# Kernel optimization log

Hardware: AMD Instinct MI355X
Metric: run time of the kernel (lower is better)

The kernel has to match this reference:

```python
import jax, jax.numpy as jnp
import numpy as np

N = 100000
E = 3200000
IN_DIM = 128
HID = 64
BN_EPS = 1e-5


def _gcn_conv(x, W, b, src, dst, dinv):
    h = x @ W                                      # [N, out]
    coeff = (dinv[src] * dinv[dst])[:, None]       # [E, 1]
    msg = h[src] * coeff                           # gather over edges
    agg = jax.ops.segment_sum(msg, dst, num_segments=N)
    agg = agg + h * (dinv * dinv)[:, None]         # self-loop term
    return agg + b


def setup_inputs() -> dict:
    key = jax.random.key(0)
    ks = jax.random.split(key, 12)
    x = jax.random.normal(ks[0], (N, IN_DIM), dtype=jnp.float32)
    edge_index = jax.random.randint(ks[1], (2, E), 0, N, dtype=jnp.int64)
    s1 = 1.0 / np.sqrt(IN_DIM)
    s2 = 1.0 / np.sqrt(HID)
    W1 = jax.random.uniform(ks[2], (IN_DIM, HID), jnp.float32, -s1, s1)
    b1 = jnp.zeros((HID,), jnp.float32)
    W2 = jax.random.uniform(ks[3], (HID, HID), jnp.float32, -s2, s2)
    b2 = jnp.zeros((HID,), jnp.float32)
    W3 = jax.random.uniform(ks[4], (HID, 1), jnp.float32, -s2, s2)
    b3 = jnp.zeros((1,), jnp.float32)
    g1 = jnp.ones((HID,), jnp.float32)
    beta1 = jnp.zeros((HID,), jnp.float32)
    m1 = 0.1 * jax.random.normal(ks[5], (HID,), jnp.float32)
    v1 = jax.random.uniform(ks[6], (HID,), jnp.float32) + 0.5
    g2 = jnp.ones((HID,), jnp.float32)
    beta2 = jnp.zeros((HID,), jnp.float32)
    m2 = 0.1 * jax.random.normal(ks[7], (HID,), jnp.float32)
    v2 = jax.random.uniform(ks[8], (HID,), jnp.float32) + 0.5
    return {"x": x, "edge_index": edge_index,
            "W1": W1, "b1": b1, "W2": W2, "b2": b2, "W3": W3, "b3": b3,
            "g1": g1, "beta1": beta1, "m1": m1, "v1": v1,
            "g2": g2, "beta2": beta2, "m2": m2, "v2": v2}


def reference(x, edge_index, W1, b1, W2, b2, W3, b3,
              g1, beta1, m1, v1, g2, beta2, m2, v2):
    src, dst = edge_index[0], edge_index[1]
    # degree with self-loops (computed on destination index, PyG convention)
    deg = jax.ops.segment_sum(jnp.ones((E,), jnp.float32), dst, num_segments=N) + 1.0
    dinv = jax.lax.rsqrt(deg)

    def bn(h, g, beta, m, v):
        return (h - m) * jax.lax.rsqrt(v + BN_EPS) * g + beta

    h = _gcn_conv(x, W1, b1, src, dst, dinv)
    h = jax.nn.relu(bn(h, g1, beta1, m1, v1))  # dropout is a no-op in eval
    h = _gcn_conv(h, W2, b2, src, dst, dinv)
    h = jax.nn.relu(bn(h, g2, beta2, m2, v2))
    h = _gcn_conv(h, W3, b3, src, dst, dinv)
    return jax.nn.sigmoid(h)  # [N, 1]
```

## Files before the change

kernel.cpp:

```cpp
#include <hip/hip_runtime.h>
#include <math.h>

#define N_NODES 100000
#define E_EDGES 3200000
#define IN_DIM_ 128
#define HID_ 64
#define BN_EPS_ 1e-5f

#define PB 250
#define CHUNK 12800
#define NBUCK 391
#define BMAX 9600

typedef __attribute__((ext_vector_type(8))) short short8;
typedef __attribute__((ext_vector_type(4))) float f32x4;
typedef __attribute__((ext_vector_type(2))) float f32x2;

__device__ inline ushort f2bf(float f) {
    union { float f; unsigned u; } c; c.f = f;
    unsigned r = c.u + 0x7fff + ((c.u >> 16) & 1);
    return (ushort)(r >> 16);
}
__device__ inline f32x2 up2(unsigned u) {
    union { unsigned u; float f; } lo, hi;
    lo.u = u << 16; hi.u = u & 0xffff0000u;
    f32x2 r; r.x = lo.f; r.y = hi.f; return r;
}

__global__ __launch_bounds__(512) void passA1_hist(const int* __restrict__ ei,
                                                   int* __restrict__ histPB) {
    __shared__ int hist[NBUCK];
    int t = threadIdx.x, b = blockIdx.x;
    for (int k = t; k < NBUCK; k += 512) hist[k] = 0;
    __syncthreads();
    int e0 = b * CHUNK, e1 = e0 + CHUNK;
    for (int e = e0 + t; e < e1; e += 512) {
        int d = ei[E_EDGES + e];
        atomicAdd(&hist[d >> 8], 1);
    }
    __syncthreads();
    for (int k = t; k < NBUCK; k += 512) histPB[k * PB + b] = hist[k];
}

__global__ __launch_bounds__(256) void scan_rows(int* __restrict__ histPB,
                                                 int* __restrict__ bucket_tot) {
    __shared__ int wsum[4];
    int k = blockIdx.x, t = threadIdx.x, lane = t & 63, wv = t >> 6;
    int v = (t < PB) ? histPB[k * PB + t] : 0;
    int s = v;
#pragma unroll
    for (int off = 1; off < 64; off <<= 1) {
        int u = __shfl_up(s, off, 64);
        if (lane >= off) s += u;
    }
    if (lane == 63) wsum[wv] = s;
    __syncthreads();
    int wbase = 0;
    for (int w = 0; w < wv; w++) wbase += wsum[w];
    if (t < PB) histPB[k * PB + t] = wbase + s - v;
    if (t == 255) bucket_tot[k] = wbase + s;
}

__global__ __launch_bounds__(512) void scan_totals(const int* __restrict__ bucket_tot,
                                                   int* __restrict__ bucket_base,
                                                   int* __restrict__ row_ptr) {
    __shared__ int wsum[8];
    int t = threadIdx.x, lane = t & 63, wv = t >> 6;
    int v = (t < NBUCK) ? bucket_tot[t] : 0;
    int s = v;
#pragma unroll
    for (int off = 1; off < 64; off <<= 1) {
        int u = __shfl_up(s, off, 64);
        if (lane >= off) s += u;
    }
    if (lane == 63) wsum[wv] = s;
    __syncthreads();
    int wbase = 0;
    for (int w = 0; w < wv; w++) wbase += wsum[w];
    if (t < NBUCK) bucket_base[t] = wbase + s - v;
    if (t == 0) {
        bucket_base[NBUCK] = E_EDGES;
        row_ptr[N_NODES] = E_EDGES;
    }
}

__global__ __launch_bounds__(512) void passA2_sorted(const int* __restrict__ ei,
                                                     const int* __restrict__ histPB,
                                                     const int* __restrict__ bucket_base,
                                                     int* __restrict__ ebuf) {
    __shared__ int sorted[CHUNK];
    __shared__ ushort bid[CHUNK];
    __shared__ int cur[NBUCK];
    __shared__ int lbase[NBUCK];
    int t = threadIdx.x, b = blockIdx.x;
    for (int k = t; k < NBUCK; k += 512) cur[k] = 0;
    __syncthreads();
    int e0 = b * CHUNK;
    for (int e = e0 + t; e < e0 + CHUNK; e += 512)
        atomicAdd(&cur[ei[E_EDGES + e] >> 8], 1);
    __syncthreads();
    if (t < 64) {
        int run = 0;
        for (int c0 = 0; c0 < NBUCK; c0 += 64) {
            int idx = c0 + t;
            int v = (idx < NBUCK) ? cur[idx] : 0;
            int s = v;
#pragma unroll
            for (int off = 1; off < 64; off <<= 1) {
                int u = __shfl_up(s, off, 64);
                if (t >= off) s += u;
            }
            if (idx < NBUCK) lbase[idx] = run + s - v;
            run += __shfl(s, 63, 64);
        }
    }
    __syncthreads();
    for (int k = t; k < NBUCK; k += 512) cur[k] = lbase[k];
    __syncthreads();
    for (int e = e0 + t; e < e0 + CHUNK; e += 512) {
        int s = ei[e];
        int d = ei[E_EDGES + e];
        int k = d >> 8;
        int pos = atomicAdd(&cur[k], 1);
        sorted[pos] = s | ((d & 255) << 17);
        bid[pos] = (ushort)k;
    }
    __syncthreads();
    for (int j = t; j < CHUNK; j += 512) {
        int k = bid[j];
        int dest = bucket_base[k] + histPB[k * PB + b] + (j - lbase[k]);
        ebuf[dest] = sorted[j];
    }
}

__global__ __launch_bounds__(256) void passB_sorted(const int* __restrict__ ebuf,
                                                    const int* __restrict__ bucket_base,
                                                    int* __restrict__ row_ptr,
                                                    int* __restrict__ csr_src,
                                                    float* __restrict__ dinv) {
    __shared__ int sorted[BMAX];
    __shared__ int hist[256];
    __shared__ int wsum[4];
    int b = blockIdx.x, t = threadIdx.x, lane = t & 63, wv = t >> 6;
    int base = bucket_base[b], end = bucket_base[b + 1];
    hist[t] = 0;
    __syncthreads();
    for (int k = base + t; k < end; k += 256)
        atomicAdd(&hist[ebuf[k] >> 17], 1);
    __syncthreads();
    int v = hist[t];
    int s = v;
#pragma unroll
    for (int off = 1; off < 64; off <<= 1) {
        int u = __shfl_up(s, off, 64);
        if (lane >= off) s += u;
    }
    if (lane == 63) wsum[wv] = s;
    __syncthreads();
    int wbase = 0;
    for (int w = 0; w < wv; w++) wbase += wsum[w];
    int excl = wbase + s - v;
    int node = b * 256 + t;
    if (node < N_NODES) {
        row_ptr[node] = base + excl;
        dinv[node] = rsqrtf((float)v + 1.0f);
    }
    __syncthreads();
    hist[t] = excl;
    __syncthreads();
    for (int k = base + t; k < end; k += 256) {
        int pv = ebuf[k];
        int pos = atomicAdd(&hist[pv >> 17], 1);
        if (pos < BMAX) sorted[pos] = pv;
        else csr_src[base + pos] = pv & 0x1FFFF;
    }
    __syncthreads();
    int cnt = end - base;
    if (cnt > BMAX) cnt = BMAX;
    for (int j = t; j < cnt; j += 256)
        csr_src[base + j] = sorted[j] & 0x1FFFF;
}

__global__ __launch_bounds__(256) void sort_rows(const int* __restrict__ row_ptr,
                                                 int* __restrict__ csr_src) {
    int wv = (blockIdx.x * 256 + threadIdx.x) >> 6;
    int lane = threadIdx.x & 63;
    if (wv >= N_NODES) return;
    int beg = row_ptr[wv], end = row_ptr[wv + 1];
    int deg = end - beg;
    if (deg <= 1 || deg > 64) return;
    int val = (lane < deg) ? csr_src[beg + lane] : 0x7FFFFFFF;
#pragma unroll
    for (int k = 2; k <= 64; k <<= 1) {
#pragma unroll
        for (int j = 32; j > 0; j >>= 1) {
            if (j >= k) continue;
            int other = __shfl_xor(val, j, 64);
            bool lower = (lane & j) == 0;
            bool asc = (lane & k) == 0;
            int mn = min(val, other), mx = max(val, other);
            val = (lower == asc) ? mn : mx;
        }
    }
    if (lane < deg) csr_src[beg + lane] = val;
}

template<bool LAST>
__global__ __launch_bounds__(256) void gather_feat(const int* __restrict__ row_ptr,
                                                   const int* __restrict__ csr_src,
                                                   const ushort* __restrict__ hs,
                                                   const float* __restrict__ dinv,
                                                   const float* __restrict__ b,
                                                   const float* __restrict__ g,
                                                   const float* __restrict__ beta,
                                                   const float* __restrict__ m,
                                                   const float* __restrict__ v,
                                                   unsigned* __restrict__ y,
                                                   const float* __restrict__ W3,
                                                   float* __restrict__ hs3, int n) {
    int wave = (blockIdx.x * 256 + threadIdx.x) >> 6;
    if ((wave << 3) >= n) return;
    int l = threadIdx.x & 63;
    int es = l >> 3, fg = l & 7;
    int i = (wave << 3) + es;
    bool rowok = i < n;
    int ic = rowok ? i : (n - 1);

    const char* Hb = (const char*)hs;
    unsigned foff = (unsigned)fg << 4;
    unsigned zoff = ((unsigned)N_NODES << 7) + foff;

    f32x2 a01 = {0.f, 0.f}, a23 = {0.f, 0.f}, a45 = {0.f, 0.f}, a67 = {0.f, 0.f};

    {
        uint4 p = *(const uint4*)(Hb + (((unsigned)ic << 7) + foff));
        a01 += up2(p.x); a23 += up2(p.y); a45 += up2(p.z); a67 += up2(p.w);
    }

    int beg = row_ptr[ic], end = row_ptr[ic + 1];
    for (int k = beg; k < end; k += 8) {
        unsigned o[8];
#pragma unroll
        for (int j = 0; j < 8; j++) {
            int kj = k + j;
            int sj = csr_src[kj < end ? kj : k];
            o[j] = (kj < end) ? (((unsigned)sj << 7) + foff) : zoff;
        }
        uint4 p[8];
#pragma unroll
        for (int j = 0; j < 8; j++) p[j] = *(const uint4*)(Hb + o[j]);
#pragma unroll
        for (int j = 0; j < 8; j++) {
            a01 += up2(p[j].x); a23 += up2(p[j].y);
            a45 += up2(p[j].z); a67 += up2(p[j].w);
        }
    }

    float a0 = a01.x, a1 = a01.y, a2 = a23.x, a3 = a23.y;
    float a4 = a45.x, a5 = a45.y, a6 = a67.x, a7 = a67.y;

    float4 bb0 = ((const float4*)b)[fg * 2],    bb1 = ((const float4*)b)[fg * 2 + 1];
    float4 gg0 = ((const float4*)g)[fg * 2],    gg1 = ((const float4*)g)[fg * 2 + 1];
    float4 be0 = ((const float4*)beta)[fg * 2], be1 = ((const float4*)beta)[fg * 2 + 1];
    float4 mm0 = ((const float4*)m)[fg * 2],    mm1 = ((const float4*)m)[fg * 2 + 1];
    float4 vv0 = ((const float4*)v)[fg * 2],    vv1 = ((const float4*)v)[fg * 2 + 1];
    float di = dinv[ic];
    float o0 = fmaxf((di * a0 + bb0.x - mm0.x) * (gg0.x * rsqrtf(vv0.x + BN_EPS_)) + be0.x, 0.f);
    float o1 = fmaxf((di * a1 + bb0.y - mm0.y) * (gg0.y * rsqrtf(vv0.y + BN_EPS_)) + be0.y, 0.f);
    float o2 = fmaxf((di * a2 + bb0.z - mm0.z) * (gg0.z * rsqrtf(vv0.z + BN_EPS_)) + be0.z, 0.f);
    float o3 = fmaxf((di * a3 + bb0.w - mm0.w) * (gg0.w * rsqrtf(vv0.w + BN_EPS_)) + be0.w, 0.f);
    float o4 = fmaxf((di * a4 + bb1.x - mm1.x) * (gg1.x * rsqrtf(vv1.x + BN_EPS_)) + be1.x, 0.f);
    float o5 = fmaxf((di * a5 + bb1.y - mm1.y) * (gg1.y * rsqrtf(vv1.y + BN_EPS_)) + be1.y, 0.f);
    float o6 = fmaxf((di * a6 + bb1.z - mm1.z) * (gg1.z * rsqrtf(vv1.z + BN_EPS_)) + be1.z, 0.f);
    float o7 = fmaxf((di * a7 + bb1.w - mm1.w) * (gg1.w * rsqrtf(vv1.w + BN_EPS_)) + be1.w, 0.f);

    if (LAST) {
        float4 w30 = ((const float4*)W3)[fg * 2], w31 = ((const float4*)W3)[fg * 2 + 1];
        float p = o0 * w30.x + o1 * w30.y + o2 * w30.z + o3 * w30.w +
                  o4 * w31.x + o5 * w31.y + o6 * w31.z + o7 * w31.w;
#pragma unroll
        for (int off = 1; off < 8; off <<= 1)
            p += __shfl_xor(p, off, 64);
        if (fg == 0 && rowok) hs3[i] = p * di;
    } else {
        if (rowok) {
            uint4 pk;
            pk.x = (unsigned)f2bf(o0) | ((unsigned)f2bf(o1) << 16);
            pk.y = (unsigned)f2bf(o2) | ((unsigned)f2bf(o3) << 16);
            pk.z = (unsigned)f2bf(o4) | ((unsigned)f2bf(o5) << 16);
            pk.w = (unsigned)f2bf(o6) | ((unsigned)f2bf(o7) << 16);
            ((uint4*)y)[(long)i * 8 + fg] = pk;
        }
    }
}

template<int K, bool BF16IN>
__global__ __launch_bounds__(256) void gemm_bf16(const void* __restrict__ Xv,
                                                 const float* __restrict__ W,
                                                 const float* __restrict__ dinv,
                                                 ushort* __restrict__ hs) {
    constexpr int KP = K + 8;
    __shared__ ushort A_lds[64][KP];
    __shared__ ushort Wt_lds[64][KP];
    int t = threadIdx.x;
    long row0 = (long)blockIdx.x * 64;

    for (int i = t; i < K * 16; i += 256) {
        float4 w4 = ((const float4*)W)[i];
        int k = i >> 4, n = (i & 15) * 4;
        Wt_lds[n + 0][k] = f2bf(w4.x);
        Wt_lds[n + 1][k] = f2bf(w4.y);
        Wt_lds[n + 2][k] = f2bf(w4.z);
        Wt_lds[n + 3][k] = f2bf(w4.w);
    }
    if (BF16IN) {
        constexpr int K2 = K / 2;
        const unsigned* X = (const unsigned*)Xv;
        for (int i = t; i < 64 * K2; i += 256) {
            int r = i / K2, c = i % K2;
            unsigned val = 0;
            long row = row0 + r;
            if (row < N_NODES) val = X[row * K2 + c];
            *(unsigned*)&A_lds[r][c * 2] = val;
        }
    } else {
        constexpr int K4 = K / 4;
        const float* X = (const float*)Xv;
        for (int i = t; i < 64 * K4; i += 256) {
            int r = i / K4, c = i % K4;
            float4 val = make_float4(0.f, 0.f, 0.f, 0.f);
            long row = row0 + r;
            if (row < N_NODES) val = ((const float4*)X)[row * K4 + c];
            int cb = c * 4;
            A_lds[r][cb + 0] = f2bf(val.x);
            A_lds[r][cb + 1] = f2bf(val.y);
            A_lds[r][cb + 2] = f2bf(val.z);
            A_lds[r][cb + 3] = f2bf(val.w);
        }
    }
    __syncthreads();

    int w = t >> 6, l = t & 63;
    int m = l & 15, quad = l >> 4;
    f32x4 acc[4];
#pragma unroll
    for (int c = 0; c < 4; c++) acc[c] = (f32x4){0.f, 0.f, 0.f, 0.f};

#pragma unroll
    for (int ch = 0; ch < K / 32; ch++) {
        short8 a = *(const short8*)&A_lds[16 * w + m][32 * ch + 8 * quad];
#pragma unroll
        for (int c = 0; c < 4; c++) {
            short8 b = *(const short8*)&Wt_lds[16 * c + m][32 * ch + 8 * quad];
            acc[c] = __builtin_amdgcn_mfma_f32_16x16x32_bf16(a, b, acc[c], 0, 0, 0);
        }
    }

#pragma unroll
    for (int r = 0; r < 4; r++) {
        long node = row0 + 16 * w + quad * 4 + r;
        if (node <= N_NODES) {
            float dv = (node < N_NODES) ? dinv[node] : 0.f;
#pragma unroll
            for (int c = 0; c < 4; c++)
                hs[node * 64 + 16 * c + m] = f2bf(acc[c][r] * dv);
        }
    }
}

__global__ __launch_bounds__(256) void gather3(const int* __restrict__ row_ptr,
                                               const int* __restrict__ csr_src,
                                               const float* __restrict__ hs3,
                                               const float* __restrict__ dinv,
                                               const float* __restrict__ b3,
                                               float* __restrict__ out, int n) {
    int i = blockIdx.x * 256 + threadIdx.x;
    if (i >= n) return;
    int beg = row_ptr[i], end = row_ptr[i + 1];
    float s0 = hs3[i], s1 = 0.f, s2 = 0.f, s3 = 0.f;
    float s4 = 0.f, s5 = 0.f, s6 = 0.f, s7 = 0.f;
    int k = beg;
    for (; k + 8 <= end; k += 8) {
        s0 += hs3[csr_src[k]];
        s1 += hs3[csr_src[k + 1]];
        s2 += hs3[csr_src[k + 2]];
        s3 += hs3[csr_src[k + 3]];
        s4 += hs3[csr_src[k + 4]];
        s5 += hs3[csr_src[k + 5]];
        s6 += hs3[csr_src[k + 6]];
        s7 += hs3[csr_src[k + 7]];
    }
    for (; k < end; k++) s0 += hs3[csr_src[k]];
    float z = dinv[i] * (((s0 + s1) + (s2 + s3)) + ((s4 + s5) + (s6 + s7))) + b3[0];
    out[i] = 1.f / (1.f + expf(-z));
}

extern "C" void kernel_launch(void* const* d_in, const int* in_sizes, int n_in,
                              void* d_out, int out_size, void* d_ws, size_t ws_size,
                              hipStream_t stream) {
    const int N = N_NODES;
    const int E = E_EDGES;

    const float* x   = (const float*)d_in[0];
    const int*   ei  = (const int*)d_in[1];
    const float* W1  = (const float*)d_in[2];
    const float* b1  = (const float*)d_in[3];
    const float* W2  = (const float*)d_in[4];
    const float* b2  = (const float*)d_in[5];
    const float* W3  = (const float*)d_in[6];
    const float* b3  = (const float*)d_in[7];
    const float* g1  = (const float*)d_in[8];
    const float* bt1 = (const float*)d_in[9];
    const float* m1  = (const float*)d_in[10];
    const float* v1  = (const float*)d_in[11];
    const float* g2  = (const float*)d_in[12];
    const float* bt2 = (const float*)d_in[13];
    const float* m2  = (const float*)d_in[14];
    const float* v2  = (const float*)d_in[15];
    float* out = (float*)d_out;

    int*    wsi         = (int*)d_ws;
    float*  dinv        = (float*)wsi;
    float*  hs3         = (float*)(wsi + (long)N);
    int*    row_ptr     = wsi + 2L * N;
    int*    histPB      = wsi + 3L * N + 16;
    int*    bucket_tot  = histPB + NBUCK * PB;
    int*    bucket_base = bucket_tot + 400;
    int*    csr_src     = bucket_base + 400;
    ushort* hsb         = (ushort*)(csr_src + (long)E);
    unsigned* yb        = (unsigned*)(csr_src + (long)E + 32L * (N + 1));
    int*    ebuf        = (int*)hsb;

    passA1_hist<<<PB, 512, 0, stream>>>(ei, histPB);
    scan_rows<<<NBUCK, 256, 0, stream>>>(histPB, bucket_tot);
    scan_totals<<<1, 512, 0, stream>>>(bucket_tot, bucket_base, row_ptr);
    passA2_sorted<<<PB, 512, 0, stream>>>(ei, histPB, bucket_base, ebuf);
    passB_sorted<<<NBUCK, 256, 0, stream>>>(ebuf, bucket_base, row_ptr, csr_src, dinv);
    sort_rows<<<(N + 3) / 4, 256, 0, stream>>>(row_ptr, csr_src);

    gemm_bf16<IN_DIM_, false><<<(N + 63) / 64, 256, 0, stream>>>(x, W1, dinv, hsb);
    gather_feat<false><<<(N + 31) / 32, 256, 0, stream>>>(row_ptr, csr_src, hsb, dinv,
                                                          b1, g1, bt1, m1, v1, yb, W3, hs3, N);
    gemm_bf16<HID_, true><<<(N + 63) / 64, 256, 0, stream>>>(yb, W2, dinv, hsb);
    gather_feat<true><<<(N + 31) / 32, 256, 0, stream>>>(row_ptr, csr_src, hsb, dinv,
                                                         b2, g2, bt2, m2, v2, yb, W3, hs3, N);
    gather3<<<(N + 255) / 256, 256, 0, stream>>>(row_ptr, csr_src, hs3, dinv, b3, out, N);
}
```

Measured before the change: 409.3 us.

## Fuse per-row source sort into CSR build and interleave 3 rows per gather lane

The separate sort_rows kernel is removed and each row's sources are bitonic-sorted in LDS inside passB_sorted before the CSR write-out, saving a kernel launch and a global read/write pass over csr_src. gather_feat now gives each 8-lane group three destination rows and walks their edge lists in eight interleaved slices, to raise memory-level parallelism and even out degree imbalance. It also sets a minimum-occupancy launch bound. The extra accumulators raise register pressure, and rows that spill past BMAX or have degree above 64 keep the same unsorted handling as before.

```diff
diff --git a/kernel.cpp b/kernel.cpp
--- a/kernel.cpp
+++ b/kernel.cpp
@@ -25,6 +25,21 @@
     union { unsigned u; float f; } lo, hi;
     lo.u = u << 16; hi.u = u & 0xffff0000u;
     f32x2 r; r.x = lo.f; r.y = hi.f; return r;
+}
+
+__device__ inline void bitonic64(int& val, int lane) {
+#pragma unroll
+    for (int k = 2; k <= 64; k <<= 1) {
+#pragma unroll
+        for (int j = 32; j > 0; j >>= 1) {
+            if (j >= k) continue;
+            int other = __shfl_xor(val, j, 64);
+            bool lower = (lane & j) == 0;
+            bool asc = (lane & k) == 0;
+            int mn = min(val, other), mx = max(val, other);
+            val = (lower == asc) ? mn : mx;
+        }
+    }
 }
 
 __global__ __launch_bounds__(512) void passA1_hist(const int* __restrict__ ei,
@@ -140,6 +155,7 @@
                                                     float* __restrict__ dinv) {
     __shared__ int sorted[BMAX];
     __shared__ int hist[256];
+    __shared__ int rbeg[257];
     __shared__ int wsum[4];
     int b = blockIdx.x, t = threadIdx.x, lane = t & 63, wv = t >> 6;
     int base = bucket_base[b], end = bucket_base[b + 1];
@@ -167,6 +183,8 @@
     }
     __syncthreads();
     hist[t] = excl;
+    rbeg[t] = excl;
+    if (t == 0) rbeg[256] = end - base;
     __syncthreads();
     for (int k = base + t; k < end; k += 256) {
         int pv = ebuf[k];
@@ -175,121 +193,132 @@
         else csr_src[base + pos] = pv & 0x1FFFF;
     }
     __syncthreads();
+    for (int r = wv; r < 256; r += 4) {
+        int rb = rbeg[r], re = rbeg[r + 1];
+        int d = re - rb;
+        if (d >= 2 && d <= 64 && re <= BMAX) {
+            int val = (lane < d) ? sorted[rb + lane] : 0x7FFFFFFF;
+            bitonic64(val, lane);
+            if (lane < d) sorted[rb + lane] = val;
+        }
+    }
+    __syncthreads();
     int cnt = end - base;
     if (cnt > BMAX) cnt = BMAX;
     for (int j = t; j < cnt; j += 256)
         csr_src[base + j] = sorted[j] & 0x1FFFF;
 }
 
-__global__ __launch_bounds__(256) void sort_rows(const int* __restrict__ row_ptr,
-                                                 int* __restrict__ csr_src) {
-    int wv = (blockIdx.x * 256 + threadIdx.x) >> 6;
-    int lane = threadIdx.x & 63;
-    if (wv >= N_NODES) return;
-    int beg = row_ptr[wv], end = row_ptr[wv + 1];
-    int deg = end - beg;
-    if (deg <= 1 || deg > 64) return;
-    int val = (lane < deg) ? csr_src[beg + lane] : 0x7FFFFFFF;
-#pragma unroll
-    for (int k = 2; k <= 64; k <<= 1) {
-#pragma unroll
-        for (int j = 32; j > 0; j >>= 1) {
-            if (j >= k) continue;
-            int other = __shfl_xor(val, j, 64);
-            bool lower = (lane & j) == 0;
-            bool asc = (lane & k) == 0;
-            int mn = min(val, other), mx = max(val, other);
-            val = (lower == asc) ? mn : mx;
-        }
-    }
-    if (lane < deg) csr_src[beg + lane] = val;
-}
-
 template<bool LAST>
-__global__ __launch_bounds__(256) void gather_feat(const int* __restrict__ row_ptr,
-                                                   const int* __restrict__ csr_src,
-                                                   const ushort* __restrict__ hs,
-                                                   const float* __restrict__ dinv,
-                                                   const float* __restrict__ b,
-                                                   const float* __restrict__ g,
-                                                   const float* __restrict__ beta,
-                                                   const float* __restrict__ m,
-                                                   const float* __restrict__ v,
-                                                   unsigned* __restrict__ y,
-                                                   const float* __restrict__ W3,
-                                                   float* __restrict__ hs3, int n) {
+__global__ __launch_bounds__(256, 4) void gather_feat(const int* __restrict__ row_ptr,
+                                                      const int* __restrict__ csr_src,
+                                                      const ushort* __restrict__ hs,
+                                                      const float* __restrict__ dinv,
+                                                      const float* __restrict__ b,
+                                                      const float* __restrict__ g,
+                                                      const float* __restrict__ beta,
+                                                      const float* __restrict__ m,
+                                                      const float* __restrict__ v,
+                                                      unsigned* __restrict__ y,
+                                                      const float* __restrict__ W3,
+                                                      float* __restrict__ hs3, int n) {
     int wave = (blockIdx.x * 256 + threadIdx.x) >> 6;
-    if ((wave << 3) >= n) return;
+    if (wave * 24 >= n) return;
     int l = threadIdx.x & 63;
     int es = l >> 3, fg = l & 7;
-    int i = (wave << 3) + es;
-    bool rowok = i < n;
-    int ic = rowok ? i : (n - 1);
 
     const char* Hb = (const char*)hs;
     unsigned foff = (unsigned)fg << 4;
     unsigned zoff = ((unsigned)N_NODES << 7) + foff;
 
-    f32x2 a01 = {0.f, 0.f}, a23 = {0.f, 0.f}, a45 = {0.f, 0.f}, a67 = {0.f, 0.f};
-
-    {
-        uint4 p = *(const uint4*)(Hb + (((unsigned)ic << 7) + foff));
-        a01 += up2(p.x); a23 += up2(p.y); a45 += up2(p.z); a67 += up2(p.w);
-    }
-
-    int beg = row_ptr[ic], end = row_ptr[ic + 1];
-    for (int k = beg; k < end; k += 8) {
-        unsigned o[8];
-#pragma unroll
-        for (int j = 0; j < 8; j++) {
-            int kj = k + j;
-            int sj = csr_src[kj < end ? kj : k];
-            o[j] = (kj < end) ? (((unsigned)sj << 7) + foff) : zoff;
-        }
-        uint4 p[8];
-#pragma unroll
-        for (int j = 0; j < 8; j++) p[j] = *(const uint4*)(Hb + o[j]);
-#pragma unroll
-        for (int j = 0; j < 8; j++) {
-            a01 += up2(p[j].x); a23 += up2(p[j].y);
-            a45 += up2(p[j].z); a67 += up2(p[j].w);
-        }
-    }
-
-    float a0 = a01.x, a1 = a01.y, a2 = a23.x, a3 = a23.y;
-    float a4 = a45.x, a5 = a45.y, a6 = a67.x, a7 = a67.y;
+    int ic[3]; bool ok[3];
+#pragma unroll
+    for (int r = 0; r < 3; r++) {
+        int i = wave * 24 + es + 8 * r;
+        ok[r] = i < n;
+        ic[r] = ok[r] ? i : (n - 1);
+    }
+
+    int beg[3], dg[3];
+#pragma unroll
+    for (int r = 0; r < 3; r++) {
+        beg[r] = row_ptr[ic[r]];
+        dg[r] = row_ptr[ic[r] + 1] - beg[r];
+    }
+
+    f32x2 a01[3], a23[3], a45[3], a67[3];
+#pragma unroll
+    for (int r = 0; r < 3; r++) {
+        uint4 p = *(const uint4*)(Hb + (((unsigned)ic[r] << 7) + foff));
+        a01[r] = up2(p.x); a23[r] = up2(p.y); a45[r] = up2(p.z); a67[r] = up2(p.w);
+    }
+
+#pragma unroll 1
+    for (int j = 0; j < 8; j++) {
+#pragma unroll
+        for (int r = 0; r < 3; r++) {
+            int e0 = (dg[r] * j) >> 3, e1 = (dg[r] * (j + 1)) >> 3;
+            const int* cs = csr_src + beg[r];
+            for (int l0 = e0; l0 < e1; l0 += 8) {
+                unsigned o[8];
+                uint4 p[8];
+#pragma unroll
+                for (int q = 0; q < 8; q++) {
+                    int kk = l0 + q;
+                    int sj = cs[kk < e1 ? kk : l0];
+                    o[q] = (kk < e1) ? (((unsigned)sj << 7) + foff) : zoff;
+                }
+#pragma unroll
+                for (int q = 0; q < 8; q++) p[q] = *(const uint4*)(Hb + o[q]);
+#pragma unroll
+                for (int q = 0; q < 8; q++) {
+                    a01[r] += up2(p[q].x); a23[r] += up2(p[q].y);
+                    a45[r] += up2(p[q].z); a67[r] += up2(p[q].w);
+                }
+            }
+        }
+    }
 
     float4 bb0 = ((const float4*)b)[fg * 2],    bb1 = ((const float4*)b)[fg * 2 + 1];
     float4 gg0 = ((const float4*)g)[fg * 2],    gg1 = ((const float4*)g)[fg * 2 + 1];
     float4 be0 = ((const float4*)beta)[fg * 2], be1 = ((const float4*)beta)[fg * 2 + 1];
     float4 mm0 = ((const float4*)m)[fg * 2],    mm1 = ((const float4*)m)[fg * 2 + 1];
     float4 vv0 = ((const float4*)v)[fg * 2],    vv1 = ((const float4*)v)[fg * 2 + 1];
-    float di = dinv[ic];
-    float o0 = fmaxf((di * a0 + bb0.x - mm0.x) * (gg0.x * rsqrtf(vv0.x + BN_EPS_)) + be0.x, 0.f);
-    float o1 = fmaxf((di * a1 + bb0.y - mm0.y) * (gg0.y * rsqrtf(vv0.y + BN_EPS_)) + be0.y, 0.f);
-    float o2 = fmaxf((di * a2 + bb0.z - mm0.z) * (gg0.z * rsqrtf(vv0.z + BN_EPS_)) + be0.z, 0.f);
-    float o3 = fmaxf((di * a3 + bb0.w - mm0.w) * (gg0.w * rsqrtf(vv0.w + BN_EPS_)) + be0.w, 0.f);
-    float o4 = fmaxf((di * a4 + bb1.x - mm1.x) * (gg1.x * rsqrtf(vv1.x + BN_EPS_)) + be1.x, 0.f);
-    float o5 = fmaxf((di * a5 + bb1.y - mm1.y) * (gg1.y * rsqrtf(vv1.y + BN_EPS_)) + be1.y, 0.f);
-    float o6 = fmaxf((di * a6 + bb1.z - mm1.z) * (gg1.z * rsqrtf(vv1.z + BN_EPS_)) + be1.z, 0.f);
-    float o7 = fmaxf((di * a7 + bb1.w - mm1.w) * (gg1.w * rsqrtf(vv1.w + BN_EPS_)) + be1.w, 0.f);
-
-    if (LAST) {
-        float4 w30 = ((const float4*)W3)[fg * 2], w31 = ((const float4*)W3)[fg * 2 + 1];
-        float p = o0 * w30.x + o1 * w30.y + o2 * w30.z + o3 * w30.w +
-                  o4 * w31.x + o5 * w31.y + o6 * w31.z + o7 * w31.w;
-#pragma unroll
-        for (int off = 1; off < 8; off <<= 1)
-            p += __shfl_xor(p, off, 64);
-        if (fg == 0 && rowok) hs3[i] = p * di;
-    } else {
-        if (rowok) {
-            uint4 pk;
-            pk.x = (unsigned)f2bf(o0) | ((unsigned)f2bf(o1) << 16);
-            pk.y = (unsigned)f2bf(o2) | ((unsigned)f2bf(o3) << 16);
-            pk.z = (unsigned)f2bf(o4) | ((unsigned)f2bf(o5) << 16);
-            pk.w = (unsigned)f2bf(o6) | ((unsigned)f2bf(o7) << 16);
-            ((uint4*)y)[(long)i * 8 + fg] = pk;
+    float r0 = gg0.x * rsqrtf(vv0.x + BN_EPS_), r1 = gg0.y * rsqrtf(vv0.y + BN_EPS_);
+    float r2 = gg0.z * rsqrtf(vv0.z + BN_EPS_), r3 = gg0.w * rsqrtf(vv0.w + BN_EPS_);
+    float r4 = gg1.x * rsqrtf(vv1.x + BN_EPS_), r5 = gg1.y * rsqrtf(vv1.y + BN_EPS_);
+    float r6 = gg1.z * rsqrtf(vv1.z + BN_EPS_), r7 = gg1.w * rsqrtf(vv1.w + BN_EPS_);
+    float4 w30 = make_float4(0.f, 0.f, 0.f, 0.f), w31 = make_float4(0.f, 0.f, 0.f, 0.f);
+    if (LAST) { w30 = ((const float4*)W3)[fg * 2]; w31 = ((const float4*)W3)[fg * 2 + 1]; }
+
+#pragma unroll
+    for (int r = 0; r < 3; r++) {
+        float di = dinv[ic[r]];
+        float o0 = fmaxf((di * a01[r].x + bb0.x - mm0.x) * r0 + be0.x, 0.f);
+        float o1 = fmaxf((di * a01[r].y + bb0.y - mm0.y) * r1 + be0.y, 0.f);
+        float o2 = fmaxf((di * a23[r].x + bb0.z - mm0.z) * r2 + be0.z, 0.f);
+        float o3 = fmaxf((di * a23[r].y + bb0.w - mm0.w) * r3 + be0.w, 0.f);
+        float o4 = fmaxf((di * a45[r].x + bb1.x - mm1.x) * r4 + be1.x, 0.f);
+        float o5 = fmaxf((di * a45[r].y + bb1.y - mm1.y) * r5 + be1.y, 0.f);
+        float o6 = fmaxf((di * a67[r].x + bb1.z - mm1.z) * r6 + be1.z, 0.f);
+        float o7 = fmaxf((di * a67[r].y + bb1.w - mm1.w) * r7 + be1.w, 0.f);
+
+        if (LAST) {
+            float p = o0 * w30.x + o1 * w30.y + o2 * w30.z + o3 * w30.w +
+                      o4 * w31.x + o5 * w31.y + o6 * w31.z + o7 * w31.w;
+#pragma unroll
+            for (int off = 1; off < 8; off <<= 1)
+                p += __shfl_xor(p, off, 64);
+            if (fg == 0 && ok[r]) hs3[ic[r]] = p * di;
+        } else {
+            if (ok[r]) {
+                uint4 pk;
+                pk.x = (unsigned)f2bf(o0) | ((unsigned)f2bf(o1) << 16);
+                pk.y = (unsigned)f2bf(o2) | ((unsigned)f2bf(o3) << 16);
+                pk.z = (unsigned)f2bf(o4) | ((unsigned)f2bf(o5) << 16);
+                pk.w = (unsigned)f2bf(o6) | ((unsigned)f2bf(o7) << 16);
+                ((uint4*)y)[(long)ic[r] * 8 + fg] = pk;
+            }
         }
     }
 }
@@ -436,13 +465,12 @@
     scan_totals<<<1, 512, 0, stream>>>(bucket_tot, bucket_base, row_ptr);
     passA2_sorted<<<PB, 512, 0, stream>>>(ei, histPB, bucket_base, ebuf);
     passB_sorted<<<NBUCK, 256, 0, stream>>>(ebuf, bucket_base, row_ptr, csr_src, dinv);
-    sort_rows<<<(N + 3) / 4, 256, 0, stream>>>(row_ptr, csr_src);
 
     gemm_bf16<IN_DIM_, false><<<(N + 63) / 64, 256, 0, stream>>>(x, W1, dinv, hsb);
-    gather_feat<false><<<(N + 31) / 32, 256, 0, stream>>>(row_ptr, csr_src, hsb, dinv,
+    gather_feat<false><<<(N + 95) / 96, 256, 0, stream>>>(row_ptr, csr_src, hsb, dinv,
                                                           b1, g1, bt1, m1, v1, yb, W3, hs3, N);
     gemm_bf16<HID_, true><<<(N + 63) / 64, 256, 0, stream>>>(yb, W2, dinv, hsb);
-    gather_feat<true><<<(N + 31) / 32, 256, 0, stream>>>(row_ptr, csr_src, hsb, dinv,
+    gather_feat<true><<<(N + 95) / 96, 256, 0, stream>>>(row_ptr, csr_src, hsb, dinv,
                                                          b2, g2, bt2, m2, v2, yb, W3, hs3, N);
     gather3<<<(N + 255) / 256, 256, 0, stream>>>(row_ptr, csr_src, hs3, dinv, b3, out, N);
 }
```

New measurement: 460.2 us. 1.12x slower.
